# Optimization experiments

Hardware: AMD Instinct MI355X
Metric: run time of the kernel (lower is better)

The kernel has to match this reference:

```python
import jax, jax.numpy as jnp
import numpy as np

HEADS = 8
DIM_HEAD = 64
NH = 16
NW = 16
SCALE = DIM_HEAD ** -0.5


def _avg2x2(a):
    # 2x2 average pool, stride 1, over axes 1,2 of [B,H,W,C] (== unfold+mean in torch)
    return (a[:, :-1, :-1] + a[:, 1:, :-1] + a[:, :-1, 1:] + a[:, 1:, 1:]) * 0.25


def _split_heads(t):
    B, n, _ = t.shape
    return t.reshape(B, n, HEADS, DIM_HEAD).transpose(0, 2, 1, 3)  # b h n d


def setup_inputs() -> dict:
    key = jax.random.key(0)
    ks = jax.random.split(key, 5)
    B, n, dim = 64, 482, 512
    inner = HEADS * DIM_HEAD
    return {
        "x": jax.random.normal(ks[0], (B, n, dim), jnp.float32),
        "mask": jax.random.normal(ks[1], (B, n, dim), jnp.float32),
        "W_qkv": jax.random.normal(ks[2], (3 * inner, dim), jnp.float32) * 0.02,
        "W_out": jax.random.normal(ks[3], (dim, inner), jnp.float32) * 0.02,
        "b_out": jax.random.normal(ks[4], (dim,), jnp.float32) * 0.02,
    }


def reference(x, mask, W_qkv, W_out, b_out):
    sg = jax.lax.stop_gradient
    B, n, dim = x.shape
    inner = HEADS * DIM_HEAD
    nHW = NH * NW            # 256
    nb = (NH - 1) * (NW - 1)  # 225

    # qkv projection
    qkv = x @ W_qkv.T                              # [B,n,3*inner]
    q, k, v = (
        _split_heads(t) for t in jnp.split(qkv, 3, axis=-1)
    )

    # mask path (no grad)
    mask_ = sg(mask)
    updated = (jnp.mean(mask_[:, 1:], axis=-1, keepdims=True) > 0.0).astype(x.dtype)
    updated = jnp.concatenate([jnp.ones_like(updated[:, :1]), updated], axis=1)  # [B,n,1]
    qkv_m = mask_ @ jnp.abs(sg(W_qkv)).T
    q_m, k_m, v_m = (_split_heads(t) for t in jnp.split(qkv_m, 3, axis=-1))
    q_m = q_m / (1e-6 + jnp.max(q_m, axis=2, keepdims=True))
    k_m = k_m / (1e-6 + jnp.max(k_m, axis=2, keepdims=True))
    v_m = v_m / (1e-6 + jnp.max(v_m, axis=2, keepdims=True))
    q_m, k_m, v_m = sg(q_m), sg(k_m), sg(v_m)

    # mask-modulated attention
    dots = jnp.einsum('bhnd,bhmd->bhnm', q * q_m, k * k_m) * SCALE
    attn = jax.nn.softmax(dots, axis=-1)
    out = jnp.einsum('bhnm,bhmd->bhnd', attn, v_m * v)
    out = out.transpose(0, 2, 1, 3).reshape(B, n, inner) * updated

    m = jnp.einsum('bhnm,bhmd->bhnd', sg(attn), v_m)
    m = sg(m.transpose(0, 2, 1, 3).reshape(B, n, inner) * updated)

    # overlap blending (is_overlap=True)
    inv_tail = 1.0 - updated[:, -nb:]
    inv_grid = 1.0 - updated[:, 1:nHW + 1]

    out_bridge = _avg2x2(out[:, 1:nHW + 1].reshape(B, NH, NW, inner)).reshape(B, nb, inner) * inv_tail
    out_origin = jnp.pad(out[:, -nb:].reshape(B, NH - 1, NW - 1, inner),
                         ((0, 0), (1, 1), (1, 1), (0, 0)))
    out_origin = _avg2x2(out_origin).reshape(B, nHW, inner) * inv_grid

    m_bridge = _avg2x2(m[:, 1:nHW + 1].reshape(B, NH, NW, inner)).reshape(B, nb, inner) * inv_tail
    m_origin = jnp.pad(m[:, -nb:].reshape(B, NH - 1, NW - 1, inner),
                       ((0, 0), (1, 1), (1, 1), (0, 0)))
    m_origin = _avg2x2(m_origin).reshape(B, nHW, inner) * inv_grid

    out = out.at[:, 1:nHW + 1].add(out_origin).at[:, -nb:].add(out_bridge)
    m = sg(m.at[:, 1:nHW + 1].add(m_origin).at[:, -nb:].add(m_bridge))

    # nearest-neighbor interpolation of mask means (no grad)
    mm = jnp.mean(m[:, 1:], axis=-1, keepdims=True)          # [B,n-1,1]
    a = mm[:, :nHW].reshape(B, 1, NH, NW)
    inter = jnp.repeat(jnp.repeat(a, 16, axis=2), 16, axis=3)  # [B,1,256,256]
    b = mm[:, -nb:].reshape(B, 1, NH - 1, NW - 1)
    inter_shift = jnp.repeat(jnp.repeat(b, 16, axis=2), 16, axis=3)  # [B,1,240,240]
    inter = inter.at[:, :, 8:-8, 8:-8].set((inter[:, :, 8:-8, 8:-8] + inter_shift) * 0.5)
    inter = sg(inter)

    m = sg(m @ jnp.abs(sg(W_out)).T)

    out_final = out @ W_out.T + b_out
    return out_final, m, inter
```

## Files before the change

### kernel.cpp

```cpp
#include <hip/hip_runtime.h>

#define B_      64
#define NSEQ    482
#define DIM     512
#define HEADS_  8
#define HD      64
#define QKV3    1536
#define NPAD    512
#define MROWS   (B_ * NSEQ)

typedef __bf16 v8bf __attribute__((ext_vector_type(8)));
typedef float  v4f  __attribute__((ext_vector_type(4)));
typedef unsigned int v4u __attribute__((ext_vector_type(4)));

typedef __attribute__((address_space(1))) const unsigned short gu16;
typedef __attribute__((address_space(3))) unsigned short lu16;

__device__ __forceinline__ unsigned short f2bf(float f) {
    unsigned u = __float_as_uint(f);
    u += 0x7fffu + ((u >> 16) & 1u);
    return (unsigned short)(u >> 16);
}
__device__ __forceinline__ float bf2f(unsigned short h) {
    return __uint_as_float(((unsigned)h) << 16);
}
__device__ __forceinline__ v8bf vabs8(v8bf x) {
    v4u u;
    __builtin_memcpy(&u, &x, 16);
    u &= (v4u){0x7fff7fffu, 0x7fff7fffu, 0x7fff7fffu, 0x7fff7fffu};
    v8bf r;
    __builtin_memcpy(&r, &u, 16);
    return r;
}

__global__ void k_cvt(const float* __restrict__ s, unsigned short* __restrict__ d, int n4) {
    int i = blockIdx.x * 256 + threadIdx.x;
    if (i < n4) {
        float4 v = ((const float4*)s)[i];
        ushort4 o;
        o.x = f2bf(v.x); o.y = f2bf(v.y); o.z = f2bf(v.z); o.w = f2bf(v.w);
        ((ushort4*)d)[i] = o;
    }
}

__global__ __launch_bounds__(256) void k_cvtmask(const float* __restrict__ mask,
                                                 unsigned short* __restrict__ mb,
                                                 float* __restrict__ upd) {
    int row = blockIdx.x * 4 + (threadIdx.x >> 6);
    int lane = threadIdx.x & 63;
    const float4* p = (const float4*)(mask + (size_t)row * DIM);
    ushort4* d = (ushort4*)(mb + (size_t)row * DIM);
    float s = 0.f;
    #pragma unroll
    for (int j = 0; j < 2; j++) {
        float4 v = p[j * 64 + lane];
        ushort4 o;
        o.x = f2bf(v.x); o.y = f2bf(v.y); o.z = f2bf(v.z); o.w = f2bf(v.w);
        d[j * 64 + lane] = o;
        s += v.x + v.y + v.z + v.w;
    }
    #pragma unroll
    for (int off = 32; off; off >>= 1) s += __shfl_xor(s, off);
    if (lane == 0) {
        int i = row % NSEQ;
        upd[row] = (i == 0) ? 1.f : ((s > 0.f) ? 1.f : 0.f);
    }
}

__global__ __launch_bounds__(256, 2) void k_gemm2(const unsigned short* __restrict__ A1,
                                                  const unsigned short* __restrict__ A2,
                                                  const unsigned short* __restrict__ Bw,
                                                  unsigned short* __restrict__ C1b,
                                                  unsigned short* __restrict__ C2b,
                                                  float* __restrict__ C1f,
                                                  float* __restrict__ C2f,
                                                  const float* __restrict__ bias,
                                                  int N, int K) {
    __shared__ __align__(16) unsigned short As1[2][128 * 32];
    __shared__ __align__(16) unsigned short As2[2][128 * 32];
    __shared__ __align__(16) unsigned short Bs[2][128 * 32];
    int tid = threadIdx.x;
    int lane = tid & 63, w = tid >> 6;
    int wm = w & 1, wn = w >> 1;
    int quad = lane >> 4, m16 = lane & 15;

    int nbx = gridDim.x, nwg = nbx * gridDim.y;
    int id = blockIdx.y * nbx + blockIdx.x;
    int q = nwg >> 3, r = nwg & 7;
    int xcd = id & 7, sub = id >> 3;
    int nid = (xcd < r ? xcd * (q + 1) : r * (q + 1) + (xcd - r) * q) + sub;
    int m0 = (nid / nbx) * 128, n0 = (nid % nbx) * 128;

    int srow = w * 16 + (lane >> 2);
    int scol = (lane & 3) * 8;
    const unsigned short* gA10 = &A1[(size_t)(m0 + srow) * K + scol];
    const unsigned short* gA11 = &A1[(size_t)(m0 + 64 + srow) * K + scol];
    const unsigned short* gA20 = &A2[(size_t)(m0 + srow) * K + scol];
    const unsigned short* gA21 = &A2[(size_t)(m0 + 64 + srow) * K + scol];
    const unsigned short* gB0  = &Bw[(size_t)(n0 + srow) * K + scol];
    const unsigned short* gB1  = &Bw[(size_t)(n0 + 64 + srow) * K + scol];
    lu16* lA10 = (lu16*)&As1[0][w * 512];
    lu16* lA11 = (lu16*)&As1[0][2048 + w * 512];
    lu16* lA20 = (lu16*)&As2[0][w * 512];
    lu16* lA21 = (lu16*)&As2[0][2048 + w * 512];
    lu16* lB0  = (lu16*)&Bs[0][w * 512];
    lu16* lB1  = (lu16*)&Bs[0][2048 + w * 512];

    v4f acc1[4][4], acc2[4][4];
    #pragma unroll
    for (int i = 0; i < 4; i++)
        #pragma unroll
        for (int j = 0; j < 4; j++) {
            acc1[i][j] = (v4f){0.f, 0.f, 0.f, 0.f};
            acc2[i][j] = (v4f){0.f, 0.f, 0.f, 0.f};
        }

    auto STAGE = [&](int bb, int s) {
        int ko = s << 5;
        int bo = bb << 12;
        __builtin_amdgcn_global_load_lds((gu16*)(gA10 + ko), lA10 + bo, 16, 0, 0);
        __builtin_amdgcn_global_load_lds((gu16*)(gA11 + ko), lA11 + bo, 16, 0, 0);
        __builtin_amdgcn_global_load_lds((gu16*)(gA20 + ko), lA20 + bo, 16, 0, 0);
        __builtin_amdgcn_global_load_lds((gu16*)(gA21 + ko), lA21 + bo, 16, 0, 0);
        __builtin_amdgcn_global_load_lds((gu16*)(gB0  + ko), lB0  + bo, 16, 0, 0);
        __builtin_amdgcn_global_load_lds((gu16*)(gB1  + ko), lB1  + bo, 16, 0, 0);
    };
    auto COMPUTE = [&](int bb) {
        v8bf a1[4], a2[4];
        #pragma unroll
        for (int i = 0; i < 4; i++) {
            a1[i] = *(const v8bf*)&As1[bb][(wm * 64 + i * 16 + m16) * 32 + quad * 8];
            a2[i] = *(const v8bf*)&As2[bb][(wm * 64 + i * 16 + m16) * 32 + quad * 8];
        }
        #pragma unroll
        for (int j = 0; j < 4; j++) {
            v8bf bf = *(const v8bf*)&Bs[bb][(wn * 64 + j * 16 + m16) * 32 + quad * 8];
            v8bf ba = vabs8(bf);
            #pragma unroll
            for (int i = 0; i < 4; i++) {
                acc1[i][j] = __builtin_amdgcn_mfma_f32_16x16x32_bf16(a1[i], bf, acc1[i][j], 0, 0, 0);
                acc2[i][j] = __builtin_amdgcn_mfma_f32_16x16x32_bf16(a2[i], ba, acc2[i][j], 0, 0, 0);
            }
        }
    };

    int steps = K >> 5;
    STAGE(0, 0);
    for (int s = 0; s < steps; s += 2) {
        __syncthreads();
        STAGE(1, s + 1);
        COMPUTE(0);
        __syncthreads();
        if (s + 2 < steps) STAGE(0, s + 2);
        COMPUTE(1);
    }

    if (C1f) {
        #pragma unroll
        for (int j = 0; j < 4; j++) {
            int col = n0 + wn * 64 + j * 16 + m16;
            float bi = bias ? bias[col] : 0.f;
            #pragma unroll
            for (int i = 0; i < 4; i++) {
                int rowb = m0 + wm * 64 + i * 16 + quad * 4;
                #pragma unroll
                for (int r = 0; r < 4; r++) {
                    size_t off = (size_t)(rowb + r) * N + col;
                    C1f[off] = acc1[i][j][r] + bi;
                    C2f[off] = acc2[i][j][r];
                }
            }
        }
    } else {
        unsigned short* wbuf = &As1[0][w * 1024];
        int rr = lane >> 2;
        int c0 = ((lane & 3) * 2) ^ ((rr >> 1) & 7);
        size_t colb = n0 + wn * 64 + (lane & 3) * 16;
        #pragma unroll
        for (int i = 0; i < 4; i++) {
            #pragma unroll
            for (int j = 0; j < 4; j++)
                #pragma unroll
                for (int r = 0; r < 4; r++) {
                    int row = quad * 4 + r;
                    int e = j * 16 + m16;
                    int es = ((((e >> 3) ^ ((row >> 1) & 7)) << 3) | (e & 7));
                    wbuf[row * 64 + es] = f2bf(acc1[i][j][r]);
                }
            int4 p0 = *(const int4*)&wbuf[rr * 64 + c0 * 8];
            int4 p1 = *(const int4*)&wbuf[rr * 64 + (c0 ^ 1) * 8];
            size_t off0 = (size_t)(m0 + wm * 64 + i * 16 + rr) * N + colb;
            *(int4*)&C1b[off0] = p0;
            *(int4*)&C1b[off0 + 8] = p1;
        }
        #pragma unroll
        for (int i = 0; i < 4; i++) {
            #pragma unroll
            for (int j = 0; j < 4; j++)
                #pragma unroll
                for (int r = 0; r < 4; r++) {
                    int row = quad * 4 + r;
                    int e = j * 16 + m16;
                    int es = ((((e >> 3) ^ ((row >> 1) & 7)) << 3) | (e & 7));
                    wbuf[row * 64 + es] = f2bf(acc2[i][j][r]);
                }
            int4 p0 = *(const int4*)&wbuf[rr * 64 + c0 * 8];
            int4 p1 = *(const int4*)&wbuf[rr * 64 + (c0 ^ 1) * 8];
            size_t off0 = (size_t)(m0 + wm * 64 + i * 16 + rr) * N + colb;
            *(int4*)&C2b[off0] = p0;
            *(int4*)&C2b[off0 + 8] = p1;
        }
    }
}

__global__ void k_colmax(const unsigned short* __restrict__ qm, float* __restrict__ invsc) {
    int b = blockIdx.x;
    int c = blockIdx.y * 256 + threadIdx.x;
    const unsigned short* p = qm + (size_t)b * NSEQ * QKV3 + c;
    float mx = -1e30f;
    for (int i = 0; i < NSEQ; i++) mx = fmaxf(mx, bf2f(p[(size_t)i * QKV3]));
    invsc[b * QKV3 + c] = 1.f / (1e-6f + mx);
}

__global__ __launch_bounds__(256) void k_build(const unsigned short* __restrict__ qkv,
                                               const unsigned short* __restrict__ qm,
                                               const float* __restrict__ invsc,
                                               unsigned short* __restrict__ QQ,
                                               unsigned short* __restrict__ KK,
                                               unsigned short* __restrict__ VVt,
                                               unsigned short* __restrict__ VMt) {
    __shared__ unsigned short tv[64][72];
    __shared__ unsigned short tm[64][72];
    int tid = threadIdx.x;
    int dd = tid & 63, il = tid >> 6;
    int it = blockIdx.x, h = blockIdx.y, b = blockIdx.z;
    int i0 = it * 64;
    size_t bh = (size_t)(b * HEADS_ + h);
    int c = h * HD + dd;
    float invq = invsc[b * QKV3 + c] * 0.125f;
    float invk = invsc[b * QKV3 + 512 + c];
    float invv = invsc[b * QKV3 + 1024 + c];
    #pragma unroll 4
    for (int p = 0; p < 16; p++) {
        int li = p * 4 + il;
        int i = i0 + li;
        unsigned short oq = 0, ok = 0, ov = 0, om = 0;
        if (i < NSEQ) {
            size_t base = ((size_t)(b * NSEQ + i)) * QKV3 + c;
            float q  = bf2f(qkv[base]),        qv = bf2f(qm[base]);
            float kk = bf2f(qkv[base + 512]),  kv = bf2f(qm[base + 512]);
            float vv = bf2f(qkv[base + 1024]), vm = bf2f(qm[base + 1024]);
            oq = f2bf(q * qv * invq);
            ok = f2bf(kk * kv * invk);
            float vmn = vm * invv;
            ov = f2bf(vv * vmn);
            om = f2bf(vmn);
        }
        QQ[(bh * NPAD + i) * HD + dd] = oq;
        KK[(bh * NPAD + i) * HD + dd] = ok;
        tv[li][dd] = ov;
        tm[li][dd] = om;
    }
    __syncthreads();
    #pragma unroll 4
    for (int p = 0; p < 16; p++) {
        int dr = p * 4 + il;
        VVt[(bh * HD + dr) * NPAD + i0 + dd] = tv[dd][dr];
        VMt[(bh * HD + dr) * NPAD + i0 + dd] = tm[dd][dr];
    }
}

__global__ __launch_bounds__(256, 3) void k_attn(const unsigned short* __restrict__ QQ,
                                                 const unsigned short* __restrict__ KK,
                                                 const unsigned short* __restrict__ VVt,
                                                 const unsigned short* __restrict__ VMt,
                                                 const float* __restrict__ upd,
                                                 float* __restrict__ OUT1,
                                                 float* __restrict__ M1) {
    __shared__ __align__(16) unsigned short Ks[2][32 * 72];
    __shared__ __align__(16) unsigned short Vs[2][64 * 40];
    __shared__ __align__(16) unsigned short Ms[2][64 * 40];
    __shared__ __align__(16) unsigned short Ps[4][32 * 40];

    int tid = threadIdx.x;
    int w = tid >> 6, lane = tid & 63;
    int quad = lane >> 4, m16 = lane & 15;
    int id = (blockIdx.z * 8 + blockIdx.y) * 4 + blockIdx.x;
    int nid = (id & 7) * 256 + (id >> 3);
    int b = nid >> 5, h = (nid >> 2) & 7;
    int q0 = (nid & 3) * 128 + w * 32;
    size_t bh = (size_t)(b * HEADS_ + h);

    v8bf aq[2][2];
    #pragma unroll
    for (int s = 0; s < 2; s++) {
        const unsigned short* qb = &QQ[(bh * NPAD + q0 + s * 16 + m16) * HD];
        aq[s][0] = *(const v8bf*)&qb[quad * 8];
        aq[s][1] = *(const v8bf*)&qb[32 + quad * 8];
    }

    v4f vacc[2][4], macc[2][4];
    #pragma unroll
    for (int s = 0; s < 2; s++)
        #pragma unroll
        for (int dt = 0; dt < 4; dt++) {
            vacc[s][dt] = (v4f){0.f, 0.f, 0.f, 0.f};
            macc[s][dt] = (v4f){0.f, 0.f, 0.f, 0.f};
        }
    float lrun[2][4];
    #pragma unroll
    for (int s = 0; s < 2; s++)
        #pragma unroll
        for (int r = 0; r < 4; r++) lrun[s][r] = 0.f;

    const unsigned short* gK = &KK[bh * NPAD * HD + tid * 8];
    const unsigned short* gV = &VVt[(bh * HD + (tid >> 2)) * NPAD + (tid & 3) * 8];
    const unsigned short* gM = &VMt[(bh * HD + (tid >> 2)) * NPAD + (tid & 3) * 8];
    int oK = (tid >> 3) * 72 + (tid & 7) * 8;
    int oV = (tid >> 2) * 40 + (tid & 3) * 8;
    unsigned short* Pw = &Ps[w][0];

    int4 rk = *(const int4*)gK;
    int4 rv = *(const int4*)gV;
    int4 rm = *(const int4*)gM;

    for (int ic = 0; ic < 16; ++ic) {
        int buf = ic & 1;
        *(int4*)&Ks[buf][oK] = rk;
        *(int4*)&Vs[buf][oV] = rv;
        *(int4*)&Ms[buf][oV] = rm;
        if (ic < 15) {
            rk = *(const int4*)(gK + (ic + 1) * 32 * HD);
            rv = *(const int4*)(gV + (ic + 1) * 32);
            rm = *(const int4*)(gM + (ic + 1) * 32);
        }
        __syncthreads();

        v8bf kf[2][2];
        #pragma unroll
        for (int t = 0; t < 2; t++) {
            kf[t][0] = *(const v8bf*)&Ks[buf][(t * 16 + m16) * 72 + quad * 8];
            kf[t][1] = *(const v8bf*)&Ks[buf][(t * 16 + m16) * 72 + 32 + quad * 8];
        }
        v4f S[2][2];
        #pragma unroll
        for (int s = 0; s < 2; s++)
            #pragma unroll
            for (int t = 0; t < 2; t++) {
                v4f a = (v4f){0.f, 0.f, 0.f, 0.f};
                a = __builtin_amdgcn_mfma_f32_16x16x32_bf16(aq[s][0], kf[t][0], a, 0, 0, 0);
                a = __builtin_amdgcn_mfma_f32_16x16x32_bf16(aq[s][1], kf[t][1], a, 0, 0, 0);
                S[s][t] = a;
            }

        int i0 = ic * 32;
        if (i0 + 32 > NSEQ) {
            bool x0 = (i0 + m16) >= NSEQ;
            bool x1 = (i0 + 16 + m16) >= NSEQ;
            #pragma unroll
            for (int s = 0; s < 2; s++)
                #pragma unroll
                for (int r = 0; r < 4; r++) {
                    if (x0) S[s][0][r] = -1e30f;
                    if (x1) S[s][1][r] = -1e30f;
                }
        }

        #pragma unroll
        for (int s = 0; s < 2; s++)
            #pragma unroll
            for (int r = 0; r < 4; r++) {
                float e0 = __expf(S[s][0][r]);
                float e1 = __expf(S[s][1][r]);
                lrun[s][r] += e0 + e1;
                Pw[(s * 16 + quad * 4 + r) * 40 + m16] = f2bf(e0);
                Pw[(s * 16 + quad * 4 + r) * 40 + 16 + m16] = f2bf(e1);
            }

        v8bf ap[2];
        ap[0] = *(const v8bf*)&Pw[m16 * 40 + quad * 8];
        ap[1] = *(const v8bf*)&Pw[(16 + m16) * 40 + quad * 8];

        #pragma unroll
        for (int dt = 0; dt < 4; dt++) {
            v8bf bv = *(const v8bf*)&Vs[buf][(dt * 16 + m16) * 40 + quad * 8];
            v8bf bm = *(const v8bf*)&Ms[buf][(dt * 16 + m16) * 40 + quad * 8];
            #pragma unroll
            for (int s = 0; s < 2; s++) {
                vacc[s][dt] = __builtin_amdgcn_mfma_f32_16x16x32_bf16(ap[s], bv, vacc[s][dt], 0, 0, 0);
                macc[s][dt] = __builtin_amdgcn_mfma_f32_16x16x32_bf16(ap[s], bm, macc[s][dt], 0, 0, 0);
            }
        }
    }

    #pragma unroll
    for (int s = 0; s < 2; s++)
        #pragma unroll
        for (int r = 0; r < 4; r++) {
            float sum = lrun[s][r];
            sum += __shfl_xor(sum, 1);
            sum += __shfl_xor(sum, 2);
            sum += __shfl_xor(sum, 4);
            sum += __shfl_xor(sum, 8);
            float iv = 1.f / sum;
            int iq = q0 + s * 16 + quad * 4 + r;
            if (iq < NSEQ) {
                float u = upd[b * NSEQ + iq] * iv;
                size_t off = ((size_t)(b * NSEQ + iq)) * DIM + h * HD + m16;
                #pragma unroll
                for (int dt = 0; dt < 4; dt++) {
                    OUT1[off + dt * 16] = vacc[s][dt][r] * u;
                    M1[off + dt * 16]   = macc[s][dt][r] * u;
                }
            }
        }
}

__global__ __launch_bounds__(256) void k_blend(const float* __restrict__ O1,
                                               const float* __restrict__ Mm,
                                               const float* __restrict__ upd,
                                               unsigned short* __restrict__ O2,
                                               unsigned short* __restrict__ M2,
                                               float* __restrict__ mm) {
    int blk = blockIdx.x;
    int b = blk / NSEQ, i = blk - b * NSEQ;
    int tid = threadIdx.x;
    size_t rb = (size_t)blk * DIM;
    int ns = 0;
    size_t src[4];
    float wgt = 0.f;
    if (i >= 1) {
        wgt = 0.25f * (1.f - upd[blk]);
        if (wgt != 0.f) {
            if (i <= 256) {
                int g = i - 1, gy = g >> 4, gx = g & 15;
                #pragma unroll
                for (int dy = 0; dy < 2; dy++)
                    #pragma unroll
                    for (int dx = 0; dx < 2; dx++) {
                        int sy = gy - 1 + dy, sx = gx - 1 + dx;
                        if (sy >= 0 && sy < 15 && sx >= 0 && sx < 15)
                            src[ns++] = ((size_t)(b * NSEQ + 257 + sy * 15 + sx)) * DIM;
                    }
            } else {
                int t = i - 257, ty = t / 15, tx = t - ty * 15;
                #pragma unroll
                for (int dy = 0; dy < 2; dy++)
                    #pragma unroll
                    for (int dx = 0; dx < 2; dx++)
                        src[ns++] = ((size_t)(b * NSEQ + 1 + (ty + dy) * 16 + (tx + dx))) * DIM;
            }
        }
    }
    float msum = 0.f;
    for (int c = tid; c < DIM; c += 256) {
        float o = O1[rb + c], m = Mm[rb + c];
        float ao = 0.f, am = 0.f;
        for (int s = 0; s < ns; s++) { ao += O1[src[s] + c]; am += Mm[src[s] + c]; }
        o += wgt * ao;
        m += wgt * am;
        O2[rb + c] = f2bf(o);
        M2[rb + c] = f2bf(m);
        msum += m;
    }
    #pragma unroll
    for (int off = 32; off; off >>= 1) msum += __shfl_xor(msum, off);
    __shared__ float red[4];
    if ((tid & 63) == 0) red[tid >> 6] = msum;
    __syncthreads();
    if (tid == 0 && i >= 1)
        mm[b * 481 + i - 1] = (red[0] + red[1] + red[2] + red[3]) * (1.f / 512.f);
}

__global__ void k_inter(const float* __restrict__ mm, float* __restrict__ dst) {
    int idx = blockIdx.x * 256 + threadIdx.x;
    int b = idx >> 16, rem = idx & 65535;
    int y = rem >> 8, x = rem & 255;
    const float* mb = mm + b * 481;
    float v = mb[((y >> 4) << 4) + (x >> 4)];
    if (y >= 8 && y < 248 && x >= 8 && x < 248)
        v = 0.5f * (v + mb[256 + ((y - 8) >> 4) * 15 + ((x - 8) >> 4)]);
    dst[idx] = v;
}

extern "C" void kernel_launch(void* const* d_in, const int* in_sizes, int n_in,
                              void* d_out, int out_size, void* d_ws, size_t ws_size,
                              hipStream_t stream) {
    const float* x    = (const float*)d_in[0];
    const float* mask = (const float*)d_in[1];
    const float* Wqkv = (const float*)d_in[2];
    const float* Wout = (const float*)d_in[3];
    const float* bout = (const float*)d_in[4];
    float* out = (float*)d_out;

    char* ws = (char*)d_ws;
    size_t o = 0;
    auto alloc = [&](size_t bytes) -> char* {
        char* r = ws + o;
        o += (bytes + 255) & ~(size_t)255;
        return r;
    };
    unsigned short* xb    = (unsigned short*)alloc((size_t)MROWS * DIM * 2);
    unsigned short* maskb = (unsigned short*)alloc((size_t)MROWS * DIM * 2);
    unsigned short* Wb    = (unsigned short*)alloc((size_t)QKV3 * DIM * 2);
    unsigned short* Wob   = (unsigned short*)alloc((size_t)DIM * DIM * 2);
    unsigned short* qkvb  = (unsigned short*)alloc((size_t)MROWS * QKV3 * 2);
    unsigned short* qkvmb = (unsigned short*)alloc((size_t)MROWS * QKV3 * 2);
    float* upd  = (float*)alloc((size_t)MROWS * 4);
    float* invs = (float*)alloc((size_t)B_ * QKV3 * 4);
    float* mm   = (float*)alloc((size_t)B_ * 481 * 4);
    unsigned short* QQ  = (unsigned short*)alloc((size_t)B_ * HEADS_ * NPAD * HD * 2);
    unsigned short* KK  = (unsigned short*)alloc((size_t)B_ * HEADS_ * NPAD * HD * 2);
    unsigned short* VVt = (unsigned short*)alloc((size_t)B_ * HEADS_ * NPAD * HD * 2);
    unsigned short* VMt = (unsigned short*)alloc((size_t)B_ * HEADS_ * NPAD * HD * 2);
    float* OUT1 = (float*)qkvb;
    float* M1p  = (float*)qkvmb;
    unsigned short* O2 = xb;
    unsigned short* M2 = maskb;

    k_cvt<<<(MROWS * DIM / 4) / 256, 256, 0, stream>>>(x, xb, MROWS * DIM / 4);
    k_cvtmask<<<MROWS / 4, 256, 0, stream>>>(mask, maskb, upd);
    k_cvt<<<(QKV3 * DIM / 4) / 256, 256, 0, stream>>>(Wqkv, Wb, QKV3 * DIM / 4);
    k_cvt<<<(DIM * DIM / 4) / 256, 256, 0, stream>>>(Wout, Wob, DIM * DIM / 4);

    dim3 g1(QKV3 / 128, MROWS / 128);
    k_gemm2<<<g1, 256, 0, stream>>>(xb, maskb, Wb, qkvb, qkvmb,
                                    nullptr, nullptr, nullptr, QKV3, DIM);

    k_colmax<<<dim3(B_, QKV3 / 256), 256, 0, stream>>>(qkvmb, invs);
    k_build<<<dim3(8, HEADS_, B_), 256, 0, stream>>>(qkvb, qkvmb, invs, QQ, KK, VVt, VMt);

    k_attn<<<dim3(4, HEADS_, B_), 256, 0, stream>>>(QQ, KK, VVt, VMt, upd, OUT1, M1p);

    k_blend<<<MROWS, 256, 0, stream>>>(OUT1, M1p, upd, O2, M2, mm);
    k_inter<<<(B_ * 65536) / 256, 256, 0, stream>>>(mm, out + (size_t)2 * MROWS * DIM);

    dim3 g2(DIM / 128, MROWS / 128);
    k_gemm2<<<g2, 256, 0, stream>>>(O2, M2, Wob, nullptr, nullptr,
                                    out, out + (size_t)MROWS * DIM, bout, DIM, DIM);
}
```

Measured before the change: 756.4 us.

## Triple-buffer GEMM LDS staging with vmcnt waits and XOR-swizzled layout

Changes the dual-output QKV GEMM from double to triple buffering. Each step now waits with a partial s_waitcnt vmcnt and a single raw barrier instead of two __syncthreads, so global-to-LDS loads for step s+2 run while step s is computed. It also XOR-swizzles the 16-byte column chunk both when staging and when reading fragments, to cut LDS bank conflicts. LDS use rises by half (about 72KB per block), which may limit occupancy under launch_bounds(256,2).

```diff
diff --git a/kernel.cpp b/kernel.cpp
--- a/kernel.cpp
+++ b/kernel.cpp
@@ -8,6 +8,7 @@
 #define QKV3    1536
 #define NPAD    512
 #define MROWS   (B_ * NSEQ)
+#define GT      4096
 
 typedef __bf16 v8bf __attribute__((ext_vector_type(8)));
 typedef float  v4f  __attribute__((ext_vector_type(4)));
@@ -76,9 +77,9 @@
                                                   float* __restrict__ C2f,
                                                   const float* __restrict__ bias,
                                                   int N, int K) {
-    __shared__ __align__(16) unsigned short As1[2][128 * 32];
-    __shared__ __align__(16) unsigned short As2[2][128 * 32];
-    __shared__ __align__(16) unsigned short Bs[2][128 * 32];
+    __shared__ __align__(16) unsigned short As1[3 * GT];
+    __shared__ __align__(16) unsigned short As2[3 * GT];
+    __shared__ __align__(16) unsigned short Bs[3 * GT];
     int tid = threadIdx.x;
     int lane = tid & 63, w = tid >> 6;
     int wm = w & 1, wn = w >> 1;
@@ -92,19 +93,19 @@
     int m0 = (nid / nbx) * 128, n0 = (nid % nbx) * 128;
 
     int srow = w * 16 + (lane >> 2);
-    int scol = (lane & 3) * 8;
+    int scol = ((lane & 3) ^ ((lane >> 2) & 3)) * 8;
     const unsigned short* gA10 = &A1[(size_t)(m0 + srow) * K + scol];
     const unsigned short* gA11 = &A1[(size_t)(m0 + 64 + srow) * K + scol];
     const unsigned short* gA20 = &A2[(size_t)(m0 + srow) * K + scol];
     const unsigned short* gA21 = &A2[(size_t)(m0 + 64 + srow) * K + scol];
     const unsigned short* gB0  = &Bw[(size_t)(n0 + srow) * K + scol];
     const unsigned short* gB1  = &Bw[(size_t)(n0 + 64 + srow) * K + scol];
-    lu16* lA10 = (lu16*)&As1[0][w * 512];
-    lu16* lA11 = (lu16*)&As1[0][2048 + w * 512];
-    lu16* lA20 = (lu16*)&As2[0][w * 512];
-    lu16* lA21 = (lu16*)&As2[0][2048 + w * 512];
-    lu16* lB0  = (lu16*)&Bs[0][w * 512];
-    lu16* lB1  = (lu16*)&Bs[0][2048 + w * 512];
+    lu16* lA10 = (lu16*)&As1[w * 512];
+    lu16* lA11 = (lu16*)&As1[2048 + w * 512];
+    lu16* lA20 = (lu16*)&As2[w * 512];
+    lu16* lA21 = (lu16*)&As2[2048 + w * 512];
+    lu16* lB0  = (lu16*)&Bs[w * 512];
+    lu16* lB1  = (lu16*)&Bs[2048 + w * 512];
 
     v4f acc1[4][4], acc2[4][4];
     #pragma unroll
@@ -115,9 +116,8 @@
             acc2[i][j] = (v4f){0.f, 0.f, 0.f, 0.f};
         }
 
-    auto STAGE = [&](int bb, int s) {
+    auto STAGE = [&](int bo, int s) {
         int ko = s << 5;
-        int bo = bb << 12;
         __builtin_amdgcn_global_load_lds((gu16*)(gA10 + ko), lA10 + bo, 16, 0, 0);
         __builtin_amdgcn_global_load_lds((gu16*)(gA11 + ko), lA11 + bo, 16, 0, 0);
         __builtin_amdgcn_global_load_lds((gu16*)(gA20 + ko), lA20 + bo, 16, 0, 0);
@@ -125,16 +125,17 @@
         __builtin_amdgcn_global_load_lds((gu16*)(gB0  + ko), lB0  + bo, 16, 0, 0);
         __builtin_amdgcn_global_load_lds((gu16*)(gB1  + ko), lB1  + bo, 16, 0, 0);
     };
-    auto COMPUTE = [&](int bb) {
+    int csw = (quad ^ (m16 & 3)) << 3;
+    auto COMPUTE = [&](int bo) {
         v8bf a1[4], a2[4];
         #pragma unroll
         for (int i = 0; i < 4; i++) {
-            a1[i] = *(const v8bf*)&As1[bb][(wm * 64 + i * 16 + m16) * 32 + quad * 8];
-            a2[i] = *(const v8bf*)&As2[bb][(wm * 64 + i * 16 + m16) * 32 + quad * 8];
+            a1[i] = *(const v8bf*)&As1[bo + (wm * 64 + i * 16 + m16) * 32 + csw];
+            a2[i] = *(const v8bf*)&As2[bo + (wm * 64 + i * 16 + m16) * 32 + csw];
         }
         #pragma unroll
         for (int j = 0; j < 4; j++) {
-            v8bf bf = *(const v8bf*)&Bs[bb][(wn * 64 + j * 16 + m16) * 32 + quad * 8];
+            v8bf bf = *(const v8bf*)&Bs[bo + (wn * 64 + j * 16 + m16) * 32 + csw];
             v8bf ba = vabs8(bf);
             #pragma unroll
             for (int i = 0; i < 4; i++) {
@@ -146,14 +147,18 @@
 
     int steps = K >> 5;
     STAGE(0, 0);
-    for (int s = 0; s < steps; s += 2) {
-        __syncthreads();
-        STAGE(1, s + 1);
-        COMPUTE(0);
-        __syncthreads();
-        if (s + 2 < steps) STAGE(0, s + 2);
-        COMPUTE(1);
-    }
+    STAGE(GT, 1);
+    int b0 = 0, b1 = GT, b2 = 2 * GT;
+    for (int s = 0; s < steps; ++s) {
+        if (s < steps - 1) asm volatile("s_waitcnt vmcnt(6)" ::: "memory");
+        else               asm volatile("s_waitcnt vmcnt(0)" ::: "memory");
+        __builtin_amdgcn_s_barrier();
+        __builtin_amdgcn_sched_barrier(0);
+        if (s + 2 < steps) STAGE(b2, s + 2);
+        COMPUTE(b0);
+        int t = b0; b0 = b1; b1 = b2; b2 = t;
+    }
+    __syncthreads();
 
     if (C1f) {
         #pragma unroll
@@ -172,7 +177,7 @@
             }
         }
     } else {
-        unsigned short* wbuf = &As1[0][w * 1024];
+        unsigned short* wbuf = &As1[w * 1024];
         int rr = lane >> 2;
         int c0 = ((lane & 3) * 2) ^ ((rr >> 1) & 7);
         size_t colb = n0 + wn * 64 + (lane & 3) * 16;
```

After: 754.3 us. About the same (-0.3%).
